# Performance work log

Hardware: AMD Instinct MI355X
Metric: run time of the kernel (lower is better)

The kernel has to match this reference:

```python
import jax, jax.numpy as jnp
import numpy as np

B, IN_DIM, Q_DIM, CODE_DIM, K, PROJ_DIM = 8192, 512, 128, 1024, 8, 64
NUM_LAYERS = 5
THRESHOLD = 0.9
SPARSITY_LEVELS = list(map(int, np.linspace(5, CODE_DIM, K)))  # matches torch default


def setup_inputs() -> dict:
    key = jax.random.key(0)
    ks = jax.random.split(key, 9)
    s = 0.02
    return {
        "x": jax.random.normal(ks[0], (B, IN_DIM), jnp.float32),
        "Wq": jax.random.normal(ks[1], (IN_DIM, Q_DIM), jnp.float32) * s,
        "bq": jnp.zeros((Q_DIM,), jnp.float32),
        "keys": jax.random.normal(ks[2], (K, Q_DIM), jnp.float32) * s,
        "We": jax.random.normal(ks[3], (K, IN_DIM, CODE_DIM), jnp.float32) * s,
        "S": jax.random.normal(ks[4], (K, CODE_DIM, CODE_DIM), jnp.float32) * s,
        "theta": jax.random.uniform(ks[5], (K,), jnp.float32) * 0.01,
        "W1": jax.random.normal(ks[6], (CODE_DIM, CODE_DIM), jnp.float32) * s,
        "b1": jnp.zeros((CODE_DIM,), jnp.float32),
        "W2": jax.random.normal(ks[7], (CODE_DIM, PROJ_DIM), jnp.float32) * s,
        "b2": jnp.zeros((PROJ_DIM,), jnp.float32),
    }


def _soft(z, theta):
    return jnp.sign(z) * jnp.maximum(jnp.abs(z) - theta, 0.0)


def reference(x, Wq, bq, keys, We, S, theta, W1, b1, W2, b2):
    # --- gating (attention): softmax(q @ keys^T / sqrt(d)) -> (B, K)
    q = x @ Wq + bq
    scores = (q @ keys.T) / jnp.sqrt(jnp.asarray(Q_DIM, x.dtype))
    gating_probs = jax.nn.softmax(scores, axis=-1)

    # --- all K LISTA experts densely: zs has shape (K, B, code_dim)
    Bx = jnp.einsum('bi,kic->kbc', x, We)            # (K, B, C)
    th = theta[:, None, None]
    z = _soft(Bx, th)
    for _ in range(NUM_LAYERS):
        z = _soft(Bx + jnp.einsum('kbc,kcd->kbd', z, S), th)

    # hard top-k (sparsity_level) magnitude pruning per expert
    pruned = []
    for k in range(K):
        zk = z[k]
        kk = SPARSITY_LEVELS[k]
        az = jnp.abs(zk)
        kth = jax.lax.top_k(az, kk)[0][:, -1]         # (B,)
        pruned.append(jnp.where(az >= kth[:, None], zk, 0.0))
    zs = jnp.stack(pruned, axis=0)                    # (K, B, C)

    # --- hard gating: among experts with p >= threshold*p_max, pick the
    # one with the smallest sparsity level (argmax always eligible, so the
    # empty-eligible branch in the torch code is unreachable for threshold<=1)
    p_max = jnp.max(gating_probs, axis=-1, keepdims=True)
    eligible = gating_probs >= THRESHOLD * p_max      # (B, K)
    sl = jnp.asarray(SPARSITY_LEVELS, jnp.float32)
    idx = jnp.argmin(jnp.where(eligible, sl[None, :], jnp.inf), axis=-1)  # (B,)

    selected_z = jnp.take_along_axis(zs, idx[None, :, None], axis=0)[0]   # (B, C)

    # --- projection head
    h = jax.nn.relu(selected_z @ W1 + b1)
    return h @ W2 + b2
```

## Files before the change

### kernel.cpp

```cpp
#include <hip/hip_runtime.h>
#include <math.h>

#define NB 8192
#define IND 512
#define QDIM 128
#define CD 1024
#define KE 8
#define PD 64
#define PCAP 160

typedef _Float16 h8 __attribute__((ext_vector_type(8)));
typedef _Float16 h4 __attribute__((ext_vector_type(4)));
typedef float fx16 __attribute__((ext_vector_type(16)));

#define GLD16(g, l) __builtin_amdgcn_global_load_lds((const __attribute__((address_space(1))) void*)(g), (__attribute__((address_space(3))) void*)(l), 16, 0, 0)

__device__ __forceinline__ float softt(float v, float th) {
    float a = fabsf(v) - th;
    return a > 0.0f ? copysignf(a, v) : 0.0f;
}

__device__ __forceinline__ void fsplit(float v, _Float16& hi, _Float16& lo) {
    hi = (_Float16)v;
    lo = (_Float16)((v - (float)hi) * 2048.0f);
}

__global__ void k_precompute_M(const float* __restrict__ Wq, const float* __restrict__ keys,
                               const float* __restrict__ bq, float* __restrict__ M,
                               float* __restrict__ sb) {
    const float RSQ = 0.088388347648318447f;
    int g = blockIdx.x * 256 + threadIdx.x;
    if (g < IND * KE) {
        int i = g >> 3, k = g & 7;
        float s = 0.f;
        for (int q = 0; q < QDIM; ++q) s += Wq[i * QDIM + q] * keys[k * QDIM + q];
        M[g] = s * RSQ;
    }
    if (blockIdx.x == 0 && threadIdx.x < KE) {
        int k = threadIdx.x;
        float s = 0.f;
        for (int q = 0; q < QDIM; ++q) s += bq[q] * keys[k * QDIM + q];
        sb[k] = s * RSQ;
    }
}

__global__ __launch_bounds__(256)
void k_scores(const float* __restrict__ x, const float* __restrict__ M,
              const float* __restrict__ sb, int* __restrict__ idx) {
    __shared__ float Ms[KE][IND];
    __shared__ float sbs[KE];
    int t = threadIdx.x;
    #pragma unroll
    for (int j = 0; j < 16; ++j) {
        int e = j * 256 + t;
        Ms[e & 7][e >> 3] = M[e];
    }
    if (t < KE) sbs[t] = sb[t];
    __syncthreads();
    int w = t >> 6, lane = t & 63;
    int row = blockIdx.x * 4 + w;
    const float* xr = x + (size_t)row * IND;
    float sc[KE];
    #pragma unroll
    for (int k = 0; k < KE; ++k) sc[k] = 0.f;
    #pragma unroll
    for (int j = 0; j < IND / 64; ++j) {
        int ii = lane + 64 * j;
        float xv = xr[ii];
        #pragma unroll
        for (int k = 0; k < KE; ++k) sc[k] += xv * Ms[k][ii];
    }
    #pragma unroll
    for (int k = 0; k < KE; ++k) {
        #pragma unroll
        for (int off = 32; off >= 1; off >>= 1) sc[k] += __shfl_down(sc[k], off, 64);
    }
    if (lane == 0) {
        float smax = -1e30f;
        #pragma unroll
        for (int k = 0; k < KE; ++k) { sc[k] += sbs[k]; smax = fmaxf(smax, sc[k]); }
        const float LN09 = -0.105360515657826301f;
        int e = 0;
        #pragma unroll
        for (int k = KE - 1; k >= 0; --k)
            if (sc[k] >= smax + LN09) e = k;
        idx[row] = e;
    }
}

__global__ __launch_bounds__(256)
void k_count(const int* __restrict__ idx, int* __restrict__ perm,
             int* __restrict__ counts, int* __restrict__ offsets) {
    __shared__ int hist[256][KE];
    __shared__ int sc[2][KE][256];
    __shared__ int base[KE];
    const int t = threadIdx.x;
    int pc[KE];
    #pragma unroll
    for (int e = 0; e < KE; ++e) pc[e] = 0;
    for (int j = 0; j < NB / 256; ++j) pc[idx[j * 256 + t]]++;
    #pragma unroll
    for (int e = 0; e < KE; ++e) { hist[t][e] = pc[e]; sc[0][e][t] = pc[e]; }
    __syncthreads();
    int cur = 0;
    for (int d = 1; d < 256; d <<= 1) {
        #pragma unroll
        for (int e = 0; e < KE; ++e) {
            int v = sc[cur][e][t];
            if (t >= d) v += sc[cur][e][t - d];
            sc[cur ^ 1][e][t] = v;
        }
        cur ^= 1;
        __syncthreads();
    }
    if (t == 0) {
        int a = 0;
        #pragma unroll
        for (int e = 0; e < KE; ++e) {
            int tot = sc[cur][e][255];
            base[e] = a; offsets[e] = a; counts[e] = tot; a += tot;
        }
    }
    __syncthreads();
    int pos[KE];
    #pragma unroll
    for (int e = 0; e < KE; ++e) pos[e] = base[e] + sc[cur][e][t] - hist[t][e];
    for (int j = 0; j < NB / 256; ++j) {
        int r = j * 256 + t;
        int e = idx[r];
        perm[pos[e]++] = r;
    }
}

__global__ __launch_bounds__(256)
void k_split_rows(const float* __restrict__ src, _Float16* __restrict__ ph,
                  _Float16* __restrict__ pl, int n) {
    int i = (blockIdx.x * 256 + threadIdx.x) * 4;
    if (i < n) {
        float4 v = *(const float4*)(src + i);
        h4 hh, ll;
        #pragma unroll
        for (int j = 0; j < 4; ++j) {
            _Float16 a, b;
            fsplit((&v.x)[j], a, b);
            hh[j] = a; ll[j] = b;
        }
        *(h4*)(ph + i) = hh;
        *(h4*)(pl + i) = ll;
    }
}

__global__ __launch_bounds__(256)
void k_tsplit(const float* __restrict__ src, _Float16* __restrict__ th,
              _Float16* __restrict__ tl, int K, const int* __restrict__ counts) {
    int e = blockIdx.z;
    if (counts[e] == 0) return;
    __shared__ float tile[64][65];
    int k0 = blockIdx.x * 64;
    int n0 = blockIdx.y * 64;
    const float* s = src + (size_t)e * K * CD;
    int t = threadIdx.x;
    int tr = t >> 4;
    int tc = (t & 15) * 4;
    #pragma unroll
    for (int p = 0; p < 4; ++p) {
        int kk = tr + p * 16;
        float4 v = *(const float4*)&s[(size_t)(k0 + kk) * CD + n0 + tc];
        #pragma unroll
        for (int j = 0; j < 4; ++j) tile[kk][tc + j] = (&v.x)[j];
    }
    __syncthreads();
    int n = t >> 2;
    int kq = (t & 3) * 16;
    h8 hh0, hh1, ll0, ll1;
    #pragma unroll
    for (int j = 0; j < 8; ++j) {
        _Float16 a, b;
        fsplit(tile[kq + j][n], a, b);
        hh0[j] = a; ll0[j] = b;
        fsplit(tile[kq + 8 + j][n], a, b);
        hh1[j] = a; ll1[j] = b;
    }
    size_t ob = ((size_t)e * CD + n0 + n) * K + k0 + kq;
    *(h8*)(th + ob) = hh0;
    *(h8*)(th + ob + 8) = hh1;
    *(h8*)(tl + ob) = ll0;
    *(h8*)(tl + ob + 8) = ll1;
}

template <int KDIM, int MODE>
__global__ __launch_bounds__(256)
void k_mfma(const _Float16* __restrict__ Ah, const _Float16* __restrict__ Al,
            const _Float16* __restrict__ Bh, const _Float16* __restrict__ Bl,
            const float* __restrict__ theta, const float* __restrict__ BxBuf,
            float* __restrict__ BxOut, _Float16* __restrict__ zh, _Float16* __restrict__ zl,
            float* __restrict__ zf,
            const int* __restrict__ perm, const int* __restrict__ counts,
            const int* __restrict__ offsets) {
    const int e = blockIdx.z;
    const int cnt = counts[e];
    const int p = blockIdx.x + 8 * blockIdx.y;
    const int gx = p & 7;
    const int qq = p >> 3;
    const int bxl = qq & 7;
    const int byl = gx + 8 * (qq >> 3);
    const int m0 = byl * 128;
    if (m0 >= cnt) return;
    const int n0 = bxl * 128;
    const int off = offsets[e];
    const float th = theta[e];

    __shared__ _Float16 Asl[2][128 * 64];
    __shared__ _Float16 Bsl[2][128 * 64];

    const int t = threadIdx.x;
    const int lane = t & 63;
    const int w = t >> 6;

    const _Float16* aptr[4];
    const _Float16* bptr[4];
    #pragma unroll
    for (int i = 0; i < 4; ++i) {
        int s = w * 4 + i;
        int r = s * 8 + (lane >> 3);
        int pc = lane & 7;
        int lc = pc ^ ((r ^ (r >> 3)) & 7);
        int comp = lc & 1;
        int kg = lc >> 1;
        int mrow = m0 + r; if (mrow > cnt - 1) mrow = cnt - 1;
        size_t grow;
        if constexpr (MODE == 0) grow = (size_t)perm[off + mrow];
        else grow = (size_t)(off + mrow);
        aptr[i] = (comp ? Al : Ah) + grow * KDIM + kg * 8;
        bptr[i] = (comp ? Bl : Bh) + ((size_t)e * CD + n0 + r) * KDIM + kg * 8;
    }

    const int wm = w >> 1, wn = w & 1;
    const int q = lane >> 5;
    const int ml = lane & 31;

    fx16 acc1[2][2], acc2[2][2];
    #pragma unroll
    for (int mt = 0; mt < 2; ++mt)
        #pragma unroll
        for (int nt = 0; nt < 2; ++nt)
            #pragma unroll
            for (int g = 0; g < 16; ++g) { acc1[mt][nt][g] = 0.f; acc2[mt][nt][g] = 0.f; }

    auto stage = [&](int kt, int buf) {
        const int koff = kt * 32;
        #pragma unroll
        for (int i = 0; i < 4; ++i) {
            GLD16(aptr[i] + koff, &Asl[buf][(w * 4 + i) * 512]);
            GLD16(bptr[i] + koff, &Bsl[buf][(w * 4 + i) * 512]);
        }
    };

    const int NT = KDIM / 32;
    stage(0, 0);
    __syncthreads();
    for (int kt = 0; kt < NT; ++kt) {
        const int buf = kt & 1;
        if (kt + 1 < NT) stage(kt + 1, buf ^ 1);
        #pragma unroll
        for (int ks = 0; ks < 2; ++ks) {
            const int base = ks * 4 + q * 2;
            h8 ah[2], al2[2], bh2[2], bl2[2];
            #pragma unroll
            for (int mt = 0; mt < 2; ++mt) {
                int row = wm * 64 + mt * 32 + ml;
                int sw = (row ^ (row >> 3)) & 7;
                int mb = row * 64;
                ah[mt]  = *(const h8*)&Asl[buf][mb + (((base + 0) ^ sw) * 8)];
                al2[mt] = *(const h8*)&Asl[buf][mb + (((base + 1) ^ sw) * 8)];
            }
            #pragma unroll
            for (int nt = 0; nt < 2; ++nt) {
                int col = wn * 64 + nt * 32 + ml;
                int sw = (col ^ (col >> 3)) & 7;
                int nb = col * 64;
                bh2[nt] = *(const h8*)&Bsl[buf][nb + (((base + 0) ^ sw) * 8)];
                bl2[nt] = *(const h8*)&Bsl[buf][nb + (((base + 1) ^ sw) * 8)];
            }
            #pragma unroll
            for (int mt = 0; mt < 2; ++mt)
                #pragma unroll
                for (int nt = 0; nt < 2; ++nt) {
                    acc1[mt][nt] = __builtin_amdgcn_mfma_f32_32x32x16_f16(ah[mt],  bh2[nt], acc1[mt][nt], 0, 0, 0);
                    acc2[mt][nt] = __builtin_amdgcn_mfma_f32_32x32x16_f16(ah[mt],  bl2[nt], acc2[mt][nt], 0, 0, 0);
                    acc2[mt][nt] = __builtin_amdgcn_mfma_f32_32x32x16_f16(al2[mt], bh2[nt], acc2[mt][nt], 0, 0, 0);
                }
        }
        __syncthreads();
    }

    const float LSC = 4.8828125e-4f;
    #pragma unroll
    for (int mt = 0; mt < 2; ++mt)
        #pragma unroll
        for (int nt = 0; nt < 2; ++nt) {
            #pragma unroll
            for (int g = 0; g < 16; ++g) {
                int rl = wm * 64 + mt * 32 + (g & 3) + 8 * (g >> 2) + 4 * q;
                int mrow = m0 + rl;
                if (mrow < cnt) {
                    int col = n0 + wn * 64 + nt * 32 + ml;
                    size_t addr = (size_t)(off + mrow) * CD + col;
                    float v = acc1[mt][nt][g] + acc2[mt][nt][g] * LSC;
                    if constexpr (MODE == 0) {
                        BxOut[addr] = v;
                        float z = softt(v, th);
                        _Float16 a, b;
                        fsplit(z, a, b);
                        zh[addr] = a; zl[addr] = b;
                    } else if constexpr (MODE == 1) {
                        float z = softt(v + BxBuf[addr], th);
                        _Float16 a, b;
                        fsplit(z, a, b);
                        zh[addr] = a; zl[addr] = b;
                    } else {
                        zf[addr] = softt(v + BxBuf[addr], th);
                    }
                }
            }
        }
}

__global__ __launch_bounds__(256)
void k_po(const float* __restrict__ z, const int* __restrict__ offsets,
          const float* __restrict__ W1, const float* __restrict__ b1,
          const float* __restrict__ W2, const float* __restrict__ b2,
          const int* __restrict__ perm, float* __restrict__ out) {
    const int SL[KE] = {5, 150, 296, 441, 587, 732, 878, 1024};
    __shared__ float vLg[4][PCAP];
    __shared__ int   iLg[4][PCAP];
    __shared__ float hSg[4][CD];
    __shared__ float prt[4][4][64];
    const int t = threadIdx.x;
    const int lane = t & 63;
    const int wv = t >> 6;
    const int slot = blockIdx.x * 4 + wv;
    float* vL = vLg[wv];
    int* iLs = iLg[wv];
    float* hS = hSg[wv];

    int k = 0;
    #pragma unroll
    for (int e = 1; e < KE; ++e)
        if (slot >= offsets[e]) k = e;
    const int lvl = SL[k];

    const float* zr = z + (size_t)slot * CD;
    float v[16];
    unsigned ab[16];
    #pragma unroll
    for (int j = 0; j < 16; ++j) {
        v[j] = zr[lane + 64 * j];
        ab[j] = __float_as_uint(fabsf(v[j]));
    }
    unsigned thr = 0;
    for (int b = 30; b >= 0; --b) {
        unsigned cand = thr | (1u << b);
        int c = 0;
        #pragma unroll
        for (int j = 0; j < 16; ++j)
            c += __popcll(__ballot(ab[j] >= cand));
        if (c >= lvl) thr = cand;
    }
    int cnt = 0;
    #pragma unroll
    for (int j = 0; j < 16; ++j) cnt += __popcll(__ballot(ab[j] >= thr));

    float h[16];
    #pragma unroll
    for (int j = 0; j < 16; ++j) h[j] = b1[lane + 64 * j];

    if (cnt <= PCAP) {
        int base = 0;
        #pragma unroll
        for (int j = 0; j < 16; ++j) {
            bool keep = ab[j] >= thr;
            unsigned long long m = __ballot(keep);
            if (keep) {
                int pos = base + __popcll(m & ((1ULL << lane) - 1));
                vL[pos] = v[j];
                iLs[pos] = lane + 64 * j;
            }
            base += __popcll(m);
        }
        __builtin_amdgcn_wave_barrier();
        for (int e = 0; e < cnt; ++e) {
            float val = vL[e];
            const float* wr = W1 + (size_t)iLs[e] * CD;
            #pragma unroll
            for (int j = 0; j < 16; ++j)
                h[j] = fmaf(val, wr[lane + 64 * j], h[j]);
        }
    } else {
        #pragma unroll
        for (int j = 0; j < 16; ++j)
            hS[lane + 64 * j] = (ab[j] >= thr) ? v[j] : 0.f;
        __builtin_amdgcn_wave_barrier();
        for (int e = 0; e < CD; ++e) {
            float val = hS[e];
            const float* wr = W1 + (size_t)e * CD;
            #pragma unroll
            for (int j = 0; j < 16; ++j)
                h[j] = fmaf(val, wr[lane + 64 * j], h[j]);
        }
        __builtin_amdgcn_wave_barrier();
    }

    #pragma unroll
    for (int j = 0; j < 16; ++j) hS[lane + 64 * j] = fmaxf(h[j], 0.f);
    __syncthreads();

    const float* w2c = W2 + lane;
    float a[4] = {0.f, 0.f, 0.f, 0.f};
    const int i0 = wv * 256;
    #pragma unroll 4
    for (int i = i0; i < i0 + 256; i += 4) {
        float w0 = w2c[(size_t)(i + 0) * PD];
        float w1 = w2c[(size_t)(i + 1) * PD];
        float w2v = w2c[(size_t)(i + 2) * PD];
        float w3 = w2c[(size_t)(i + 3) * PD];
        #pragma unroll
        for (int r = 0; r < 4; ++r) {
            float4 hv = *(const float4*)&hSg[r][i];
            a[r] = fmaf(hv.x, w0, a[r]);
            a[r] = fmaf(hv.y, w1, a[r]);
            a[r] = fmaf(hv.z, w2v, a[r]);
            a[r] = fmaf(hv.w, w3, a[r]);
        }
    }
    #pragma unroll
    for (int r = 0; r < 4; ++r) prt[wv][r][lane] = a[r];
    __syncthreads();

    float acc = ((prt[0][wv][lane] + prt[1][wv][lane]) +
                 (prt[2][wv][lane] + prt[3][wv][lane])) + b2[lane];
    out[(size_t)perm[slot] * PD + lane] = acc;
}

extern "C" void kernel_launch(void* const* d_in, const int* in_sizes, int n_in,
                              void* d_out, int out_size, void* d_ws, size_t ws_size,
                              hipStream_t stream) {
    const float* x     = (const float*)d_in[0];
    const float* Wq    = (const float*)d_in[1];
    const float* bq    = (const float*)d_in[2];
    const float* keys  = (const float*)d_in[3];
    const float* We    = (const float*)d_in[4];
    const float* S     = (const float*)d_in[5];
    const float* theta = (const float*)d_in[6];
    const float* W1    = (const float*)d_in[7];
    const float* b1    = (const float*)d_in[8];
    const float* W2    = (const float*)d_in[9];
    const float* b2    = (const float*)d_in[10];
    float* out = (float*)d_out;

    const size_t F = (size_t)NB * CD;
    float* Bx = (float*)d_ws;
    _Float16* zAh = (_Float16*)(Bx + F);
    _Float16* zAl = zAh + F;
    float* R1 = (float*)(zAl + F);
    _Float16* xh  = (_Float16*)R1;
    _Float16* xl  = xh + (size_t)NB * IND;
    _Float16* weh = xl + (size_t)NB * IND;
    _Float16* wel = weh + (size_t)KE * IND * CD;
    _Float16* zBh = (_Float16*)R1;
    _Float16* zBl = zBh + F;
    float* z1 = R1;
    _Float16* sth = (_Float16*)(R1 + F);
    _Float16* stl = sth + F;
    float* M  = (float*)(stl + F);
    float* sb = M + IND * KE;
    int* idx     = (int*)(sb + 8);
    int* perm    = idx + NB;
    int* counts  = perm + NB;
    int* offsets = counts + KE;

    k_precompute_M<<<16, 256, 0, stream>>>(Wq, keys, bq, M, sb);
    k_scores<<<NB / 4, 256, 0, stream>>>(x, M, sb, idx);
    k_count<<<1, 256, 0, stream>>>(idx, perm, counts, offsets);

    k_split_rows<<<(NB * IND) / 1024, 256, 0, stream>>>(x, xh, xl, NB * IND);
    {
        dim3 g(IND / 64, CD / 64, KE);
        k_tsplit<<<g, 256, 0, stream>>>(We, weh, wel, IND, counts);
    }
    {
        dim3 g(CD / 64, CD / 64, KE);
        k_tsplit<<<g, 256, 0, stream>>>(S, sth, stl, CD, counts);
    }

    dim3 gg(CD / 128, NB / 128, KE);
    k_mfma<IND, 0><<<gg, 256, 0, stream>>>(xh, xl, weh, wel, theta, nullptr, Bx, zAh, zAl, nullptr, perm, counts, offsets);
    k_mfma<CD, 1><<<gg, 256, 0, stream>>>(zAh, zAl, sth, stl, theta, Bx, nullptr, zBh, zBl, nullptr, perm, counts, offsets);
    k_mfma<CD, 1><<<gg, 256, 0, stream>>>(zBh, zBl, sth, stl, theta, Bx, nullptr, zAh, zAl, nullptr, perm, counts, offsets);
    k_mfma<CD, 1><<<gg, 256, 0, stream>>>(zAh, zAl, sth, stl, theta, Bx, nullptr, zBh, zBl, nullptr, perm, counts, offsets);
    k_mfma<CD, 1><<<gg, 256, 0, stream>>>(zBh, zBl, sth, stl, theta, Bx, nullptr, zAh, zAl, nullptr, perm, counts, offsets);
    k_mfma<CD, 2><<<gg, 256, 0, stream>>>(zAh, zAl, sth, stl, theta, Bx, nullptr, nullptr, nullptr, z1, perm, counts, offsets);

    k_po<<<NB / 4, 256, 0, stream>>>(z1, offsets, W1, b1, W2, b2, perm, out);
}
```

Baseline: 621.6 us.

## Use single accumulator with pre-scaled hi operands and deeper async LDS prefetch

Merges the two fp16-split accumulators into one by scaling the hi operands by 2^-11 in fp16 before the cross-term MFMAs. This halves accumulator registers so launch_bounds can request two blocks per SM. The loop also gets a prefetch distance of two with explicit vmcnt/lgkmcnt waits and raw barriers, so global-to-LDS loads overlap more MFMA work. Scaling fp16 values by 2^-11 can push small hi values into subnormals or underflow, which may lose precision in the low-order correction terms.

```diff
diff --git a/kernel.cpp b/kernel.cpp
--- a/kernel.cpp
+++ b/kernel.cpp
@@ -189,7 +189,7 @@
 }
 
 template <int KDIM, int MODE>
-__global__ __launch_bounds__(256)
+__global__ __launch_bounds__(256, 2)
 void k_mfma(const _Float16* __restrict__ Ah, const _Float16* __restrict__ Al,
             const _Float16* __restrict__ Bh, const _Float16* __restrict__ Bl,
             const float* __restrict__ theta, const float* __restrict__ BxBuf,
@@ -239,13 +239,13 @@
     const int q = lane >> 5;
     const int ml = lane & 31;
 
-    fx16 acc1[2][2], acc2[2][2];
+    fx16 acc[2][2];
     #pragma unroll
     for (int mt = 0; mt < 2; ++mt)
         #pragma unroll
         for (int nt = 0; nt < 2; ++nt)
             #pragma unroll
-            for (int g = 0; g < 16; ++g) { acc1[mt][nt][g] = 0.f; acc2[mt][nt][g] = 0.f; }
+            for (int g = 0; g < 16; ++g) acc[mt][nt][g] = 0.f;
 
     auto stage = [&](int kt, int buf) {
         const int koff = kt * 32;
@@ -256,45 +256,69 @@
         }
     };
 
+    const _Float16 SC = (_Float16)4.8828125e-4f;
+
     const int NT = KDIM / 32;
     stage(0, 0);
-    __syncthreads();
+    stage(1, 1);
+    asm volatile("s_waitcnt vmcnt(8)" ::: "memory");
+    __builtin_amdgcn_sched_barrier(0);
+    __builtin_amdgcn_s_barrier();
+
     for (int kt = 0; kt < NT; ++kt) {
         const int buf = kt & 1;
-        if (kt + 1 < NT) stage(kt + 1, buf ^ 1);
+        h8 ah[2][2], al2[2][2], bh2[2][2], bl2[2][2];
         #pragma unroll
         for (int ks = 0; ks < 2; ++ks) {
             const int base = ks * 4 + q * 2;
-            h8 ah[2], al2[2], bh2[2], bl2[2];
             #pragma unroll
             for (int mt = 0; mt < 2; ++mt) {
                 int row = wm * 64 + mt * 32 + ml;
                 int sw = (row ^ (row >> 3)) & 7;
                 int mb = row * 64;
-                ah[mt]  = *(const h8*)&Asl[buf][mb + (((base + 0) ^ sw) * 8)];
-                al2[mt] = *(const h8*)&Asl[buf][mb + (((base + 1) ^ sw) * 8)];
+                ah[ks][mt]  = *(const h8*)&Asl[buf][mb + (((base + 0) ^ sw) * 8)];
+                al2[ks][mt] = *(const h8*)&Asl[buf][mb + (((base + 1) ^ sw) * 8)];
             }
             #pragma unroll
             for (int nt = 0; nt < 2; ++nt) {
                 int col = wn * 64 + nt * 32 + ml;
                 int sw = (col ^ (col >> 3)) & 7;
                 int nb = col * 64;
-                bh2[nt] = *(const h8*)&Bsl[buf][nb + (((base + 0) ^ sw) * 8)];
-                bl2[nt] = *(const h8*)&Bsl[buf][nb + (((base + 1) ^ sw) * 8)];
+                bh2[ks][nt] = *(const h8*)&Bsl[buf][nb + (((base + 0) ^ sw) * 8)];
+                bl2[ks][nt] = *(const h8*)&Bsl[buf][nb + (((base + 1) ^ sw) * 8)];
             }
+        }
+        asm volatile("s_waitcnt lgkmcnt(0)" ::: "memory");
+        __builtin_amdgcn_sched_barrier(0);
+        __builtin_amdgcn_s_barrier();
+        if (kt + 2 < NT) stage(kt + 2, buf);
+        #pragma unroll
+        for (int ks = 0; ks < 2; ++ks) {
+            h8 ahs[2], bhs[2];
+            #pragma unroll
+            for (int mt = 0; mt < 2; ++mt) ahs[mt] = ah[ks][mt] * SC;
+            #pragma unroll
+            for (int nt = 0; nt < 2; ++nt) bhs[nt] = bh2[ks][nt] * SC;
             #pragma unroll
             for (int mt = 0; mt < 2; ++mt)
                 #pragma unroll
                 for (int nt = 0; nt < 2; ++nt) {
-                    acc1[mt][nt] = __builtin_amdgcn_mfma_f32_32x32x16_f16(ah[mt],  bh2[nt], acc1[mt][nt], 0, 0, 0);
-                    acc2[mt][nt] = __builtin_amdgcn_mfma_f32_32x32x16_f16(ah[mt],  bl2[nt], acc2[mt][nt], 0, 0, 0);
-                    acc2[mt][nt] = __builtin_amdgcn_mfma_f32_32x32x16_f16(al2[mt], bh2[nt], acc2[mt][nt], 0, 0, 0);
+                    acc[mt][nt] = __builtin_amdgcn_mfma_f32_32x32x16_f16(ah[ks][mt],  bh2[ks][nt], acc[mt][nt], 0, 0, 0);
+                    acc[mt][nt] = __builtin_amdgcn_mfma_f32_32x32x16_f16(ahs[mt],     bl2[ks][nt], acc[mt][nt], 0, 0, 0);
+                    acc[mt][nt] = __builtin_amdgcn_mfma_f32_32x32x16_f16(al2[ks][mt], bhs[nt],     acc[mt][nt], 0, 0, 0);
                 }
         }
-        __syncthreads();
-    }
-
-    const float LSC = 4.8828125e-4f;
+        if (kt + 1 < NT) {
+            if (kt + 2 < NT) {
+                asm volatile("s_waitcnt vmcnt(8)" ::: "memory");
+            } else {
+                asm volatile("s_waitcnt vmcnt(0)" ::: "memory");
+            }
+            __builtin_amdgcn_sched_barrier(0);
+            __builtin_amdgcn_s_barrier();
+        }
+    }
+
     #pragma unroll
     for (int mt = 0; mt < 2; ++mt)
         #pragma unroll
@@ -306,7 +330,7 @@
                 if (mrow < cnt) {
                     int col = n0 + wn * 64 + nt * 32 + ml;
                     size_t addr = (size_t)(off + mrow) * CD + col;
-                    float v = acc1[mt][nt][g] + acc2[mt][nt][g] * LSC;
+                    float v = acc[mt][nt][g];
                     if constexpr (MODE == 0) {
                         BxOut[addr] = v;
                         float z = softt(v, th);
```

Measured after the change: 620.5 us. Within noise of the previous version (-0.2%).
